# Optimization experiments

Hardware: AMD Instinct MI355X
Metric: run time of the kernel (lower is better)

## Reference

```python
import jax, jax.numpy as jnp
import numpy as np

NEG = -1e9  # acts as -inf in the DP while staying finite for grads


def nw_value(theta, A):
    """Soft Needleman-Wunsch terminal value with softmax (logsumexp) operator.
    theta: [N, M] match scores; A: scalar gap score.
    Recurrence: V[i,j] = theta[i-1,j-1] + logsumexp(V[i-1,j]+A, V[i-1,j-1], V[i,j-1]+A)
    with V[0,0]=0 and V[i,0]=V[0,j]=-inf.
    """
    N, M = theta.shape
    init_row = jnp.full((M + 1,), NEG, theta.dtype).at[0].set(0.0)

    def row_step(prev_row, theta_row):
        def col_step(v_left, inp):
            th, v_diag, v_up = inp
            v = th + jnp.logaddexp(jnp.logaddexp(v_up + A, v_diag), v_left + A)
            return v, v
        _, row = jax.lax.scan(
            col_step, jnp.asarray(NEG, theta.dtype),
            (theta_row, prev_row[:-1], prev_row[1:]))
        new_row = jnp.concatenate([jnp.full((1,), NEG, theta.dtype), row])
        return new_row, None

    last_row, _ = jax.lax.scan(row_step, init_row, theta)
    return last_row[M]


def nw_decode(theta, A):
    # Soft alignment matrix = dV/dtheta (expected alignment under softmax operator),
    # matching NeedlemanWunschDecoder.decode.
    return jax.grad(nw_value)(theta, A)


def setup_inputs() -> dict:
    key = jax.random.key(0)
    ks = jax.random.split(key, 7)
    B, N, M = 8, 1024, 1024
    n_alpha, n_input, n_embed = 22, 512, 512
    x = jax.random.randint(ks[0], (B, N), 0, n_alpha)
    y = jax.random.randint(ks[1], (B, M), 0, n_alpha)
    emb = jax.random.normal(ks[2], (n_alpha, n_input), jnp.float32)
    W = jax.random.normal(ks[3], (n_input, n_embed), jnp.float32) / np.sqrt(n_input)
    b = jax.random.normal(ks[4], (n_embed,), jnp.float32) * 0.01
    Wg = jax.random.normal(ks[5], (2 * n_embed, 1), jnp.float32) / np.sqrt(2 * n_embed)
    bg = jax.random.normal(ks[6], (1,), jnp.float32) * 0.01
    return {"x": x, "y": y, "emb": emb, "W": W, "b": b, "Wg": Wg, "bg": bg}


def reference(x, y, emb, W, b, Wg, bg):
    zx = emb[x] @ W + b                       # [B, N, d] embedding (EmbedLinear)
    zy = emb[y] @ W + b                       # [B, M, d]
    theta = jnp.einsum('bid,bjd->bij', zx, zy)   # [B, N, M] pairwise match scores
    merged = jnp.concatenate([zx.mean(axis=1), zy.mean(axis=1)], axis=1)  # [B, 2d]
    A = merged @ Wg + bg                      # [B, 1] gap score
    aln = jax.vmap(nw_decode)(theta, A[:, 0])    # [B, N, M]
    return jnp.swapaxes(aln, 1, 2)               # [B, M, N] (decode(...).T per batch)
```

## Files before the change

### kernel.cpp

```cpp
#include <hip/hip_runtime.h>
#include <cstdint>
#include <cstddef>

#define NEGV -1.0e9f
#define NB 4
#define BW 4

__device__ __forceinline__ float lse_f(float a, float b) {
    float d = a - b;
    float m = fmaxf(a, b);
    return m + log1pf(expf(-fabsf(d)));
}
__device__ __forceinline__ float cellfwd(float th, float vu, float vdg, float vl, float A) {
    float inner = lse_f(vu + A, vdg);
    float outer = lse_f(inner, vl + A);
    return th + outer;
}

__device__ __forceinline__ void diag_geo(int d, int& st, int& L, int& tlo) {
    if (d < 64)        { st = (d * (d + 1)) >> 1;       L = d + 1;      tlo = 0; }
    else if (d < 1024) { st = 2080 + ((d - 64) << 6);   L = 64;         tlo = 0; }
    else               { int u = d - 1024;
                         st = 63520 + (u << 6) - ((u * (u + 1)) >> 1);
                         L = 63 - u;                    tlo = u + 1; }
}

__global__ void k_embed(const float* __restrict__ emb, const float* __restrict__ W,
                        const float* __restrict__ b, double* __restrict__ T) {
    int idx = blockIdx.x * blockDim.x + threadIdx.x;
    if (idx >= 22 * 512) return;
    int a = idx >> 9, d = idx & 511;
    double acc = (double)b[d];
    const float* er = emb + a * 512;
    for (int k = 0; k < 512; ++k) acc += (double)er[k] * (double)W[k * 512 + d];
    T[idx] = acc;
}

__global__ void k_gau(const double* __restrict__ T, const int* __restrict__ x,
                      const int* __restrict__ y, const float* __restrict__ Wg,
                      const float* __restrict__ bg,
                      double* __restrict__ G, double* __restrict__ Aout) {
    __shared__ double u1s[22], u2s[22];
    int t = threadIdx.x;
    if (t < 484) {
        int a = t / 22, c = t % 22;
        const double* ra = T + a * 512;
        const double* rc = T + c * 512;
        double acc = 0.0;
        for (int d = 0; d < 512; ++d) acc += ra[d] * rc[d];
        G[t] = acc;
    }
    if (t < 22) {
        double acc = 0.0;
        const double* ra = T + t * 512;
        for (int d = 0; d < 512; ++d) acc += ra[d] * (double)Wg[d];
        u1s[t] = acc;
    } else if (t >= 64 && t < 86) {
        int a = t - 64;
        double acc = 0.0;
        const double* ra = T + a * 512;
        for (int d = 0; d < 512; ++d) acc += ra[d] * (double)Wg[512 + d];
        u2s[a] = acc;
    }
    __syncthreads();
    int w = t >> 6, lane = t & 63;
    const int* xb = x + w * 1024;
    const int* yb = y + w * 1024;
    double s = 0.0;
    for (int i = lane; i < 1024; i += 64) s += u1s[xb[i]] + u2s[yb[i]];
    for (int off = 32; off > 0; off >>= 1) s += __shfl_down(s, off);
    if (lane == 0) Aout[w] = s * (1.0 / 1024.0) + (double)bg[0];
}

__global__ void k_vinit(float* __restrict__ Vbuf, int* __restrict__ gflag) {
    int b = blockIdx.x, t = threadIdx.x;
    float* Vb = Vbuf + (size_t)b * (1025 * 1025);
    Vb[t] = (t == 0) ? 0.0f : NEGV;
    if (t == 0) Vb[1024] = NEGV;
    Vb[(size_t)(t + 1) * 1025] = NEGV;
    if (b == 0 && t < 64) gflag[t] = 0;
}

__global__ __launch_bounds__(256) void k_fwds(const int* __restrict__ x,
                                              const int* __restrict__ y,
                                              const double* __restrict__ G,
                                              const double* __restrict__ Aarr,
                                              float* __restrict__ Vbuf,
                                              int* __restrict__ gflag) {
    __shared__ float Gs[484];
    __shared__ int ys_s[1024];
    __shared__ float topbuf[BW][1024];
    __shared__ int prog[BW];

    const int bid = blockIdx.x;
    const int b = bid & 7;
    const int p = bid >> 3;
    const int tid = threadIdx.x;
    const int w = tid >> 6;
    const int t = tid & 63;
    const int grow = (p << 8) + tid;
    float* Vb = Vbuf + (size_t)b * (1025 * 1025);

    for (int q = tid; q < 484; q += 256) Gs[q] = (float)G[q];
    for (int q = tid; q < 1024; q += 256) ys_s[q] = y[(b << 10) + q];
    if (tid < BW) prog[tid] = 0;
    const int xs = x[(b << 10) + grow];
    __syncthreads();

    const float A = (float)Aarr[b];
    const float* Grow = Gs + xs * 22;
    float* vst = Vb + (size_t)(grow + 1) * 1025 + 1;
    const float* tsrc = Vb + (size_t)(p << 8) * 1025;

    float vp = NEGV;
    float vdgc = (p == 0 && tid == 0) ? 0.0f : NEGV;
    float chunkv = NEGV;
    int cbase = 0;

    for (int s = 0; s < 1024 + 63; ++s) {
        if (w == 0 && p > 0 && s < 1024 && (s & 63) == 0) {
            while (__hip_atomic_load(&gflag[(b << 2) + p - 1], __ATOMIC_ACQUIRE,
                                     __HIP_MEMORY_SCOPE_AGENT) < s + 64)
                __builtin_amdgcn_s_sleep(2);
            chunkv = tsrc[s + 1 + t];
            cbase = s;
        }
        if (w > 0 && s < 1024 && (s & 15) == 0) {
            const int target = (s + 16 < 1024) ? s + 16 : 1024;
            while (__hip_atomic_load(&prog[w], __ATOMIC_ACQUIRE,
                                     __HIP_MEMORY_SCOPE_WORKGROUP) < target)
                __builtin_amdgcn_s_sleep(1);
        }
        float vu_l0;
        if (w == 0)
            vu_l0 = (p == 0) ? NEGV : __shfl(chunkv, s - cbase);
        else
            vu_l0 = topbuf[w][(s < 1024) ? s : 1023];
        const float ush = __shfl_up(vp, 1);
        const int j = s - t + 1;
        if (j >= 1 && j <= 1024) {
            float vu = (t == 0) ? vu_l0 : ush;
            float v = cellfwd(Grow[ys_s[j - 1]], vu, vdgc, vp, A);
            vst[j - 1] = v;
            if (t == 63) {
                if (w < BW - 1) {
                    topbuf[w + 1][j - 1] = v;
                    if ((j & 15) == 0)
                        __hip_atomic_store(&prog[w + 1], j, __ATOMIC_RELEASE,
                                           __HIP_MEMORY_SCOPE_WORKGROUP);
                } else if (p < NB - 1) {
                    if ((j & 63) == 0) {
                        __threadfence();
                        __hip_atomic_store(&gflag[(b << 2) + p], j,
                                           __ATOMIC_RELEASE, __HIP_MEMORY_SCOPE_AGENT);
                    }
                }
            }
            vp = v; vdgc = vu;
        }
    }
}

__global__ __launch_bounds__(256) void k_wb(const double* __restrict__ Aarr,
                                            const float* __restrict__ Vbuf,
                                            float* __restrict__ bw) {
    int idx = blockIdx.x * 256 + threadIdx.x;
    int b = idx >> 20;
    int cell = idx & 1048575;
    int i = (cell >> 10) + 1;
    int j = (cell & 1023) + 1;
    const float* Vb = Vbuf + (size_t)b * (1025 * 1025);
    float vu  = Vb[(size_t)(i - 1) * 1025 + j];
    float vdg = Vb[(size_t)(i - 1) * 1025 + (j - 1)];
    float vl  = Vb[(size_t)i * 1025 + (j - 1)];
    float A = (float)Aarr[b];
    float t1 = vu + A;
    float t2 = vl + A;
    float di = t1 - vdg;
    float inner = (di > 0.f) ? (t1  + log1pf(expf(-di)))
                             : (vdg + log1pf(expf(di)));
    float dw = inner - t2;
    float outer = (dw > 0.f) ? (inner + log1pf(expf(-dw)))
                             : (t2    + log1pf(expf(dw)));
    float go1 = expf(inner - outer);
    float wlW = expf(t2 - outer);
    float wuW = go1 * expf(t1 - inner);
    float wdW = go1 * expf(vdg - inner);
    float* bbp = bw + (size_t)b * 3145728;

    if (i >= 2) {
        int rb = (i - 2) >> 4, q = (i - 2) & 15, cj = j - 1;
        int st, L, tlo; diag_geo(rb + cj, st, L, tlo);
        int f = 3 * q;
        bbp[(size_t)st * 48 + (size_t)(f >> 2) * 4 * L + ((rb - tlo) << 2) + (f & 3)] = wuW;
    }
    if (i >= 2 && j >= 2) {
        int rb = (i - 2) >> 4, q = (i - 2) & 15, cj = j - 2;
        int st, L, tlo; diag_geo(rb + cj, st, L, tlo);
        int f = 3 * q + 1;
        bbp[(size_t)st * 48 + (size_t)(f >> 2) * 4 * L + ((rb - tlo) << 2) + (f & 3)] = wdW;
    }
    if (j >= 2) {
        int rb = (i - 1) >> 4, q = (i - 1) & 15, cj = j - 2;
        int st, L, tlo; diag_geo(rb + cj, st, L, tlo);
        int f = 3 * q + 2;
        bbp[(size_t)st * 48 + (size_t)(f >> 2) * 4 * L + ((rb - tlo) << 2) + (f & 3)] = wlW;
    }
}

__global__ __launch_bounds__(64) void k_bwd16(const float* __restrict__ bw,
                                              float* __restrict__ out) {
    const int t = threadIdx.x;
    const int b = blockIdx.x;
    const float* bb = bw + (size_t)b * 3145728;
    float* ob = out + ((size_t)b << 20);
    const int r0 = t << 4;

    float e[16];
    float4 cwv[12], pfv[12];
    #pragma unroll
    for (int q = 0; q < 16; ++q) e[q] = 0.f;

    {
        int st, L, tlo; diag_geo(t + 1023, st, L, tlo);
        const float* base = bb + (size_t)st * 48;
        #pragma unroll
        for (int k = 0; k < 12; ++k)
            cwv[k] = *(const float4*)(base + (size_t)k * 4 * L);
    }

    float sdb = 0.f;
    for (int s = 0; s < 1087; ++s) {
        float dn = __shfl_down(e[0], 1);
        const int d = 1086 - s;
        const int cj = d - t;
        if (cj >= 0 && cj < 1024) {
            {
                int st, L, tlo; diag_geo(d - 1, st, L, tlo);
                const int p = t - tlo;
                const float* base = bb + (size_t)st * 48 + ((size_t)p << 2);
                #pragma unroll
                for (int k = 0; k < 12; ++k)
                    pfv[k] = *(const float4*)(base + (size_t)k * 4 * L);
            }
            const float* F = (const float*)cwv;

            float old_b = e[15];
            float eu = (t == 63) ? 0.f : dn;
            float ed = (t == 63) ? 0.f : sdb;
            float v = eu * F[45] + ed * F[46] + old_b * F[47];
            if (t == 63 && cj == 1023) v = 1.0f;
            e[15] = v;
            float new_b = v;
            #pragma unroll
            for (int q = 14; q >= 0; --q) {
                float oq = e[q];
                v = new_b * F[3 * q] + old_b * F[3 * q + 1] + oq * F[3 * q + 2];
                e[q] = v;
                new_b = v; old_b = oq;
            }
            #pragma unroll
            for (int k = 0; k < 4; ++k)
                *(float4*)&ob[(size_t)cj * 1024 + r0 + 4 * k] =
                    make_float4(e[4*k], e[4*k+1], e[4*k+2], e[4*k+3]);
            #pragma unroll
            for (int k = 0; k < 12; ++k) cwv[k] = pfv[k];
        }
        sdb = dn;
    }
}

template <bool FAITHFUL>
__global__ __launch_bounds__(1024) void k_dp(const int* __restrict__ x,
                                             const int* __restrict__ y,
                                             const double* __restrict__ G,
                                             const double* __restrict__ Aarr,
                                             float2* __restrict__ wbuf,
                                             float* __restrict__ wdbuf,
                                             float* __restrict__ out) {
    __shared__ float Gs[484];
    __shared__ int xs[1024], ys[1024];
    __shared__ float D[3][1025];
    __shared__ float E[3][1026];

    const int b = blockIdx.x;
    const int t = threadIdx.x;
    const int i = t + 1;

    if (t < 484) Gs[t] = (float)G[t];
    xs[t] = x[(b << 10) + t];
    ys[t] = y[(b << 10) + t];
    D[0][t + 1] = NEGV;
    D[1][t + 1] = NEGV;
    E[0][t] = 0.f; E[1][t] = 0.f; E[2][t] = 0.f;
    if (t == 0) {
        D[0][0] = 0.0f;
        D[1][0] = NEGV;
        E[0][1024] = 0.f; E[0][1025] = 0.f;
        E[1][1024] = 0.f; E[1][1025] = 0.f;
        E[2][1024] = 0.f; E[2][1025] = 0.f;
    }
    __syncthreads();

    const float A = (float)Aarr[b];
    const float* Grow = Gs + xs[t] * 22;
    float2* wb = wbuf + ((size_t)b << 20);
    float*  wdb = wdbuf + ((size_t)b << 20);

    for (int k = 2; k <= 2048; ++k) {
        const int cur = k % 3, p1 = (k + 2) % 3, p2 = (k + 1) % 3;
        const int j = k - i;
        if (j >= 1 && j <= 1024) {
            float vu  = D[p1][i - 1];
            float vdg = D[p2][i - 1];
            float vl  = D[p1][i];
            float t1 = vu + A;
            float t2 = vl + A;
            float di = t1 - vdg;
            float inner = (di > 0.f) ? (t1  + log1pf(expf(-di)))
                                     : (vdg + log1pf(expf(di)));
            float dw = inner - t2;
            float outer = (dw > 0.f) ? (inner + log1pf(expf(-dw)))
                                     : (t2    + log1pf(expf(dw)));
            D[cur][i] = Grow[ys[j - 1]] + outer;
            float go1 = expf(inner - outer);
            float wlW = expf(t2 - outer);
            float wuW = go1 * expf(t1 - inner);
            size_t ci = ((size_t)t << 10) + (j - 1);
            wb[ci] = make_float2(wuW, wlW);
            if (FAITHFUL) wdb[ci] = go1 * expf(vdg - inner);
        }
        if (t == 0) D[cur][0] = NEGV;
        if (i == k && k <= 1024) D[cur][k] = NEGV;
        __syncthreads();
    }

    __syncthreads();

    float* ob = out + ((size_t)b << 20);

    for (int k = 2048; k >= 2; --k) {
        const int cur = k % 3, n1 = (k + 1) % 3, n2 = (k + 2) % 3;
        const int j = k - i;
        if (j >= 1 && j <= 1024) {
            float e;
            if (k == 2048) {
                e = 1.0f;
            } else {
                float Eu = E[n1][i + 1];
                float Ed = E[n2][i + 1];
                float El = E[n1][i];
                int iw = (i < 1024) ? i : 1023;
                int jw = (j < 1024) ? j : 1023;
                float2 w_up = wb[((size_t)iw << 10) + (j - 1)];
                float2 w_lf = wb[((size_t)(i - 1) << 10) + jw];
                float w_dd;
                if (FAITHFUL) {
                    w_dd = wdb[((size_t)iw << 10) + jw];
                } else {
                    float2 w_dg = wb[((size_t)iw << 10) + jw];
                    w_dd = 1.0f - w_dg.x - w_dg.y;
                }
                e = Eu * w_up.x + Ed * w_dd + El * w_lf.y;
            }
            E[cur][i] = e;
            ob[((size_t)(j - 1) << 10) + (i - 1)] = e;
        } else {
            E[cur][i] = 0.f;
        }
        __syncthreads();
    }
}

extern "C" void kernel_launch(void* const* d_in, const int* in_sizes, int n_in,
                              void* d_out, int out_size, void* d_ws, size_t ws_size,
                              hipStream_t stream) {
    const int*   x   = (const int*)d_in[0];
    const int*   y   = (const int*)d_in[1];
    const float* emb = (const float*)d_in[2];
    const float* W   = (const float*)d_in[3];
    const float* b   = (const float*)d_in[4];
    const float* Wg  = (const float*)d_in[5];
    const float* bg  = (const float*)d_in[6];
    float* out = (float*)d_out;

    char* ws = (char*)d_ws;
    double* T    = (double*)(ws + 0);
    double* G    = (double*)(ws + 90112);
    double* Aarr = (double*)(ws + 94336);
    float*  bund = (float*)(ws + 131072);
    float2* wbuf = (float2*)(ws + 131072);
    float*  wdbuf = (float*)(ws + 131072 + ((size_t)64 << 20));
    float*  Vbuf = (float*)(ws + 131072 + ((size_t)96 << 20));
    int*    gflag = (int*)(ws + 131072 + ((size_t)96 << 20) + (size_t)8 * 1025 * 1025 * 4);

    k_embed<<<44, 256, 0, stream>>>(emb, W, b, T);
    k_gau<<<1, 512, 0, stream>>>(T, x, y, Wg, bg, G, Aarr);

    const size_t need_old = 131072 + ((size_t)96 << 20);
    const size_t need_new = need_old + (size_t)8 * 1025 * 1025 * 4 + 4096;

    if (ws_size >= need_new) {
        k_vinit<<<8, 1024, 0, stream>>>(Vbuf, gflag);
        k_fwds<<<8 * NB, 256, 0, stream>>>(x, y, G, Aarr, Vbuf, gflag);
        k_wb<<<8 * 1024 * 1024 / 256, 256, 0, stream>>>(Aarr, Vbuf, bund);
        k_bwd16<<<8, 64, 0, stream>>>(bund, out);
    } else if (ws_size >= need_old) {
        k_dp<true><<<8, 1024, 0, stream>>>(x, y, G, Aarr, wbuf, wdbuf, out);
    } else {
        k_dp<false><<<8, 1024, 0, stream>>>(x, y, G, Aarr, wbuf, wdbuf, out);
    }
}
```

Baseline: 2.603 ms.

## Software-pipeline the forward NW wavefront by splitting the logsumexp into two stages

The forward DP kernel now splits each cell's update into an inner logsumexp over the up and diagonal neighbours and an outer logsumexp with the left neighbour. The inner term for the next column is computed one step ahead, while the outer term for the current column completes. The skew between lanes grows from one to two columns per row, so each step's serial dependency holds only one logsumexp instead of two. In exchange the wavefront needs more steps (about 1535 instead of 1087), and the row-boundary feed and synchronisation logic for lane 0 becomes more involved.

```diff
diff --git a/kernel.cpp b/kernel.cpp
--- a/kernel.cpp
+++ b/kernel.cpp
@@ -10,11 +10,6 @@
     float d = a - b;
     float m = fmaxf(a, b);
     return m + log1pf(expf(-fabsf(d)));
-}
-__device__ __forceinline__ float cellfwd(float th, float vu, float vdg, float vl, float A) {
-    float inner = lse_f(vu + A, vdg);
-    float outer = lse_f(inner, vl + A);
-    return th + outer;
 }
 
 __device__ __forceinline__ void diag_geo(int d, int& st, int& L, int& tlo) {
@@ -112,52 +107,91 @@
     float* vst = Vb + (size_t)(grow + 1) * 1025 + 1;
     const float* tsrc = Vb + (size_t)(p << 8) * 1025;
 
-    float vp = NEGV;
-    float vdgc = (p == 0 && tid == 0) ? 0.0f : NEGV;
-    float chunkv = NEGV;
-    int cbase = 0;
-
-    for (int s = 0; s < 1024 + 63; ++s) {
-        if (w == 0 && p > 0 && s < 1024 && (s & 63) == 0) {
-            while (__hip_atomic_load(&gflag[(b << 2) + p - 1], __ATOMIC_ACQUIRE,
-                                     __HIP_MEMORY_SCOPE_AGENT) < s + 64)
-                __builtin_amdgcn_s_sleep(2);
-            chunkv = tsrc[s + 1 + t];
-            cbase = s;
-        }
-        if (w > 0 && s < 1024 && (s & 15) == 0) {
-            const int target = (s + 16 < 1024) ? s + 16 : 1024;
+    float cur_vu = NEGV, prev_vu = NEGV;
+    if (t == 0) {
+        if (w == 0) {
+            if (p == 0) { cur_vu = NEGV; prev_vu = 0.0f; }
+            else {
+                while (__hip_atomic_load(&gflag[(b << 2) + p - 1], __ATOMIC_ACQUIRE,
+                                         __HIP_MEMORY_SCOPE_AGENT) < 64)
+                    __builtin_amdgcn_s_sleep(2);
+                prev_vu = tsrc[0];
+                cur_vu  = tsrc[1];
+            }
+        } else {
             while (__hip_atomic_load(&prog[w], __ATOMIC_ACQUIRE,
-                                     __HIP_MEMORY_SCOPE_WORKGROUP) < target)
+                                     __HIP_MEMORY_SCOPE_WORKGROUP) < 16)
                 __builtin_amdgcn_s_sleep(1);
-        }
-        float vu_l0;
-        if (w == 0)
-            vu_l0 = (p == 0) ? NEGV : __shfl(chunkv, s - cbase);
-        else
-            vu_l0 = topbuf[w][(s < 1024) ? s : 1023];
-        const float ush = __shfl_up(vp, 1);
-        const int j = s - t + 1;
-        if (j >= 1 && j <= 1024) {
-            float vu = (t == 0) ? vu_l0 : ush;
-            float v = cellfwd(Grow[ys_s[j - 1]], vu, vdgc, vp, A);
-            vst[j - 1] = v;
+            prev_vu = NEGV;
+            cur_vu  = topbuf[w][0];
+        }
+    }
+
+    float vp = NEGV, vp2 = NEGV, inner_c = 0.f;
+
+    for (int s = -1; s <= 1533; ++s) {
+        const int jo = s - 2 * tid + 1;
+        const int ji = jo + 1;
+        const float sh_vu = __shfl_up(vp, 1);
+        const float sh_vd = __shfl_up(vp2, 1);
+
+        float inner_n = 0.f;
+        const bool ji_act = (ji >= 1) && (ji <= 1024);
+        if (ji_act) {
+            float vu_i, vdg_i;
+            if (t == 0) {
+                vu_i = cur_vu; vdg_i = prev_vu;
+                if (ji < 1024) {
+                    float nxt;
+                    if (w == 0) {
+                        if (p == 0) nxt = NEGV;
+                        else {
+                            if ((ji & 63) == 0) {
+                                int tgt = ji + 64; if (tgt > 1024) tgt = 1024;
+                                while (__hip_atomic_load(&gflag[(b << 2) + p - 1],
+                                        __ATOMIC_ACQUIRE, __HIP_MEMORY_SCOPE_AGENT) < tgt)
+                                    __builtin_amdgcn_s_sleep(2);
+                            }
+                            nxt = tsrc[ji + 1];
+                        }
+                    } else {
+                        if ((ji & 15) == 0) {
+                            int tgt = ji + 16; if (tgt > 1024) tgt = 1024;
+                            while (__hip_atomic_load(&prog[w], __ATOMIC_ACQUIRE,
+                                    __HIP_MEMORY_SCOPE_WORKGROUP) < tgt)
+                                __builtin_amdgcn_s_sleep(1);
+                        }
+                        nxt = topbuf[w][ji];
+                    }
+                    prev_vu = cur_vu; cur_vu = nxt;
+                }
+            } else {
+                vu_i = sh_vu; vdg_i = sh_vd;
+            }
+            inner_n = lse_f(vu_i + A, vdg_i);
+        }
+
+        if (jo >= 1 && jo <= 1024) {
+            float outer = lse_f(inner_c, vp + A);
+            float v = Grow[ys_s[jo - 1]] + outer;
+            vst[jo - 1] = v;
             if (t == 63) {
                 if (w < BW - 1) {
-                    topbuf[w + 1][j - 1] = v;
-                    if ((j & 15) == 0)
-                        __hip_atomic_store(&prog[w + 1], j, __ATOMIC_RELEASE,
+                    topbuf[w + 1][jo - 1] = v;
+                    if ((jo & 15) == 0)
+                        __hip_atomic_store(&prog[w + 1], jo, __ATOMIC_RELEASE,
                                            __HIP_MEMORY_SCOPE_WORKGROUP);
                 } else if (p < NB - 1) {
-                    if ((j & 63) == 0) {
+                    if ((jo & 63) == 0) {
                         __threadfence();
-                        __hip_atomic_store(&gflag[(b << 2) + p], j,
+                        __hip_atomic_store(&gflag[(b << 2) + p], jo,
                                            __ATOMIC_RELEASE, __HIP_MEMORY_SCOPE_AGENT);
                     }
                 }
             }
-            vp = v; vdgc = vu;
-        }
+            vp2 = vp; vp = v;
+        }
+        inner_c = inner_n;
     }
 }
 
```

After: 3.735 ms. +43.5%, slower.

## Process two columns per thread per wavefront step in forward DP

Applied to the files above, without the earlier changes.

Each thread now computes two adjacent cells of its row per step, so the wavefront sweep takes about half as many iterations (512+63 instead of 1024+63). This cuts the per-step overhead of shuffles, branches and sync checks, and shortens the pipeline fill and drain in each wave. The cost is a serial dependency between the two cells inside a step, plus retuned polling granularity for the inter-wave and inter-block flags.

```diff
diff --git a/kernel.cpp b/kernel.cpp
--- a/kernel.cpp
+++ b/kernel.cpp
@@ -112,51 +112,67 @@
     float* vst = Vb + (size_t)(grow + 1) * 1025 + 1;
     const float* tsrc = Vb + (size_t)(p << 8) * 1025;
 
-    float vp = NEGV;
-    float vdgc = (p == 0 && tid == 0) ? 0.0f : NEGV;
+    float cA = NEGV, cB = NEGV;
+    float sdiag = (p == 0 && w == 0 && t == 0) ? 0.0f : NEGV;
     float chunkv = NEGV;
     int cbase = 0;
 
-    for (int s = 0; s < 1024 + 63; ++s) {
-        if (w == 0 && p > 0 && s < 1024 && (s & 63) == 0) {
+    for (int s = 0; s < 512 + 63; ++s) {
+        if (w == 0 && p > 0 && s < 512 && (s & 31) == 0) {
+            int tgt = 2 * s + 64; if (tgt > 1024) tgt = 1024;
             while (__hip_atomic_load(&gflag[(b << 2) + p - 1], __ATOMIC_ACQUIRE,
-                                     __HIP_MEMORY_SCOPE_AGENT) < s + 64)
+                                     __HIP_MEMORY_SCOPE_AGENT) < tgt)
                 __builtin_amdgcn_s_sleep(2);
-            chunkv = tsrc[s + 1 + t];
+            chunkv = tsrc[2 * s + 1 + t];
             cbase = s;
         }
-        if (w > 0 && s < 1024 && (s & 15) == 0) {
-            const int target = (s + 16 < 1024) ? s + 16 : 1024;
+        if (w > 0 && s < 512 && (s & 7) == 0) {
+            int tgt = 2 * s + 16; if (tgt > 1024) tgt = 1024;
             while (__hip_atomic_load(&prog[w], __ATOMIC_ACQUIRE,
-                                     __HIP_MEMORY_SCOPE_WORKGROUP) < target)
+                                     __HIP_MEMORY_SCOPE_WORKGROUP) < tgt)
                 __builtin_amdgcn_s_sleep(1);
         }
-        float vu_l0;
-        if (w == 0)
-            vu_l0 = (p == 0) ? NEGV : __shfl(chunkv, s - cbase);
-        else
-            vu_l0 = topbuf[w][(s < 1024) ? s : 1023];
-        const float ush = __shfl_up(vp, 1);
-        const int j = s - t + 1;
-        if (j >= 1 && j <= 1024) {
-            float vu = (t == 0) ? vu_l0 : ush;
-            float v = cellfwd(Grow[ys_s[j - 1]], vu, vdgc, vp, A);
-            vst[j - 1] = v;
+        const float shA = __shfl_up(cA, 1);
+        const float shB = __shfl_up(cB, 1);
+        const int cidx = (2 * (s - cbase)) & 62;
+        const float ckA = __shfl(chunkv, cidx);
+        const float ckB = __shfl(chunkv, cidx + 1);
+        const int q = s - t;
+        if (q >= 0 && q < 512) {
+            const int jA = 2 * q + 1, jB = jA + 1;
+            float vuA, vuB;
+            if (t == 0) {
+                if (w == 0) {
+                    if (p == 0) { vuA = NEGV; vuB = NEGV; }
+                    else        { vuA = ckA;  vuB = ckB;  }
+                } else {
+                    vuA = topbuf[w][jA - 1];
+                    vuB = topbuf[w][jB - 1];
+                }
+            } else { vuA = shA; vuB = shB; }
+            const float thA = Grow[ys_s[jA - 1]];
+            const float thB = Grow[ys_s[jB - 1]];
+            float vA = cellfwd(thA, vuA, sdiag, cB, A);
+            float vB = cellfwd(thB, vuB, vuA, vA, A);
+            vst[jA - 1] = vA;
+            vst[jB - 1] = vB;
             if (t == 63) {
                 if (w < BW - 1) {
-                    topbuf[w + 1][j - 1] = v;
-                    if ((j & 15) == 0)
-                        __hip_atomic_store(&prog[w + 1], j, __ATOMIC_RELEASE,
+                    topbuf[w + 1][jA - 1] = vA;
+                    topbuf[w + 1][jB - 1] = vB;
+                    if ((jB & 15) == 0)
+                        __hip_atomic_store(&prog[w + 1], jB, __ATOMIC_RELEASE,
                                            __HIP_MEMORY_SCOPE_WORKGROUP);
                 } else if (p < NB - 1) {
-                    if ((j & 63) == 0) {
+                    if ((jB & 63) == 0) {
                         __threadfence();
-                        __hip_atomic_store(&gflag[(b << 2) + p], j,
+                        __hip_atomic_store(&gflag[(b << 2) + p], jB,
                                            __ATOMIC_RELEASE, __HIP_MEMORY_SCOPE_AGENT);
                     }
                 }
             }
-            vp = v; vdgc = vu;
+            sdiag = vuB;
+            cA = vA; cB = vB;
         }
     }
 }
```

Measured after the change: 3.044 ms. 17.0% more time.
